# Kernel optimization log

Hardware: AMD Instinct MI355X
Metric: run time of the kernel (lower is better)

## Reference

```python
import jax, jax.numpy as jnp
import numpy as np

N_STATIONS = 35
N_PER_ST = 12
N_NODES = N_STATIONS * N_PER_ST   # 420
MAX_EDGES = 5120                  # true edge count = 34 * 12^2 = 4896
MAX_SUPER = 65536                 # true superedge candidates = 33*12*144 = 57024
PI = float(np.pi)

# constraint rows (r, phi, z) from the torch module
C_LO = jnp.array([269.0, -3.15, -2386.0], dtype=jnp.float32)
C_HI = jnp.array([581.0, 3.15, 2386.0], dtype=jnp.float32)


def _calc_dphi(p1, p2):
    d = p2 - p1
    d = jnp.where(d > PI, d - 2.0 * PI, d)
    return jnp.where(d < -PI, d + 2.0 * PI, d)


def _norm_node(v, k):
    return 2.0 * (v - C_LO[k]) / (C_HI[k] - C_LO[k]) - 1.0


def _norm_edge(v, k):
    return 2.0 * v / (C_HI[k] - C_LO[k])


def setup_inputs() -> dict:
    rng = np.random.default_rng(0)
    r = rng.uniform(270.0, 580.0, N_NODES)
    phi = rng.uniform(-3.1, 3.1, N_NODES)
    z = rng.uniform(-2000.0, 2000.0, N_NODES)
    station = np.arange(N_NODES) // N_PER_ST
    track = np.arange(N_NODES) % N_PER_ST  # one hit per track per station
    data = np.stack([
        np.zeros(N_NODES),          # event
        r * np.sin(phi),            # x (so atan2(x, y) = phi)
        r * np.cos(phi),            # y
        z,                          # z
        station.astype(np.float64),
        track.astype(np.float64),
        np.arange(N_NODES, dtype=np.float64),  # index_old
    ], axis=1).astype(np.float32)
    return {"event_data": jnp.asarray(data)}


def reference(event_data):
    x, y, z = event_data[:, 1], event_data[:, 2], event_data[:, 3]
    station, track, index_old = event_data[:, 4], event_data[:, 5], event_data[:, 6]
    # convert() : cartesian -> cylindrical (x<-r, y<-phi)
    r = jnp.sqrt(x * x + y * y)
    phi = jnp.arctan2(x, y)
    # get_graph(): adjacency of consecutive stations, row-major nonzero like torch
    adj = station[:, None] == (station[None, :] - 1.0)
    i_idx, j_idx = jnp.nonzero(adj, size=MAX_EDGES, fill_value=0)
    e_valid = jnp.arange(MAX_EDGES) < jnp.sum(adj)
    phi_p, phi_c = phi[i_idx], phi[j_idx]
    z_p, z_c = z[i_idx], z[j_idx]
    r_p, r_c = r[i_idx], r[j_idx]
    io_p, io_c = index_old[i_idx], index_old[j_idx]
    is_true = track[i_idx] == track[j_idx]  # torch leaves is_true uninitialized; defined as same-track
    dphi = _calc_dphi(phi_p, phi_c)
    dz, dx = z_c - z_p, r_c - r_p
    ez = (station[i_idx] + 1.0) / N_STATIONS
    e_index = jnp.arange(MAX_EDGES, dtype=event_data.dtype)
    # normalize() node-mode on endpoint phi/z (the only normalized cols used later) and edge-mode on dx,dy,dz
    yp_n, yc_n = _norm_node(phi_p, 1), _norm_node(phi_c, 1)
    zp_n, zc_n = _norm_node(z_p, 2), _norm_node(z_c, 2)
    dx_n, dy_n, dz_n = _norm_edge(dx, 0), _norm_edge(dphi, 1), _norm_edge(dz, 2)
    # apply_edge_restriction (masking instead of compaction)
    e_keep = e_valid & (dy_n > -10.0) & (dy_n < 10.0) & (dz_n > -10.0) & (dz_n < 10.0)
    # get_edges_from_supernodes: join first.index_old_c == second.index_old_p
    eq = (io_c[:, None] == io_p[None, :]) & e_keep[:, None] & e_keep[None, :]
    si, sj = jnp.nonzero(eq, size=MAX_SUPER, fill_value=0)
    s_valid = jnp.arange(MAX_SUPER) < jnp.sum(eq)
    d_first = jnp.stack([dx_n[si], dy_n[si], dz_n[si]], -1)
    d_second = jnp.stack([dx_n[sj], dy_n[sj], dz_n[sj]], -1)
    weight = jnp.linalg.norm(d_first - d_second, axis=1)
    # apply_weight_restriction: compact, order-preserving
    s_keep = s_valid & (weight < 0.1)
    (k_idx,) = jnp.nonzero(s_keep, size=MAX_SUPER, fill_value=0)
    k_valid = jnp.arange(MAX_SUPER) < jnp.sum(s_keep)
    fi, se = si[k_idx], sj[k_idx]
    su_is_true = is_true[fi] & is_true[se]
    su_ioc = jnp.where(k_valid, e_index[fi], -2.0)  # superedge index_old_c = first edge's index
    su_iop = jnp.where(k_valid, e_index[se], -2.0)  # superedge index_old_p = second edge's index
    su_y = jnp.where(k_valid, su_is_true.astype(event_data.dtype), 0.0)
    # construct_output_graph: nodes = (filtered) edges, edges = superedges
    node_idx = jnp.where(e_keep, e_index, -1.0)
    X = jnp.where(e_keep[:, None], jnp.stack([yp_n, yc_n, zp_n, zc_n, ez], -1), 0.0)
    Ri = node_idx[:, None] == su_ioc[None, :]   # [MAX_EDGES, MAX_SUPER] bool
    Ro = node_idx[:, None] == su_iop[None, :]
    super_ids = jnp.stack([su_iop, su_ioc], -1)
    edge_ids = jnp.where(e_keep[:, None], jnp.stack([io_p, io_c, e_index], -1), -1.0)
    return X, Ri, Ro, su_y, super_ids, node_idx, edge_ids
```

## Files before the change

kernel.cpp:

```cpp
#include <hip/hip_runtime.h>
#include <math.h>

#define NND 420
#define MAXE 5120
#define MAXS 65536

#define OFF_X    ((size_t)0)
#define OFF_RI   ((size_t)25600)
#define OFF_RO   ((size_t)25600 + 335544320)
#define OFF_SUY  ((size_t)671114240)
#define OFF_SIDS ((size_t)671179776)
#define OFF_NIDX ((size_t)671310848)
#define OFF_EIDS ((size_t)671315968)
#define OUT_TOTAL ((size_t)671331328)

static __device__ __forceinline__ float f32(double d) { return (float)d; }

__device__ float g_dxn[MAXE], g_dyn[MAXE], g_dzn[MAXE];
__device__ float g_iop[MAXE], g_ioc[MAXE];
__device__ int   g_keep[MAXE], g_istrue[MAXE], g_jn[MAXE];
__device__ int   g_estart[NND + 1];
__device__ int   g_cnt2[MAXE], g_off2[MAXE];
__device__ int   g_nedges, g_nkeep;

__global__ __launch_bounds__(256) void kFill(float4* __restrict__ p, size_t n4) {
    size_t i = (size_t)blockIdx.x * 256 + threadIdx.x;
    size_t stride = (size_t)gridDim.x * 256;
    const float4 z = make_float4(0.f, 0.f, 0.f, 0.f);
    for (; i < n4; i += stride) p[i] = z;
}

__global__ __launch_bounds__(512) void kA(const float* __restrict__ ev,
                                          float* __restrict__ out) {
    __shared__ float s_r[NND], s_phi[NND], s_z[NND], s_st[NND], s_trk[NND], s_io[NND];
    __shared__ int   s_cnt[NND];
    __shared__ int   s_off[NND + 1];
    __shared__ short s_ei[MAXE], s_ej[MAXE];

    const float PI_F  = f32(3.141592653589793);
    const float TPI_F = f32(6.283185307179586);
    const float LO1 = -3.15f, SPAN1 = 3.15f + 3.15f;
    const float LO2 = -2386.0f, SPAN2 = 4772.0f;
    const float SPAN0 = 312.0f;

    int t = threadIdx.x;
    for (int n = t; n < NND; n += 512) {
        float x = ev[n * 7 + 1], y = ev[n * 7 + 2];
        s_z[n]   = ev[n * 7 + 3];
        s_st[n]  = ev[n * 7 + 4];
        s_trk[n] = ev[n * 7 + 5];
        s_io[n]  = ev[n * 7 + 6];
        s_r[n]   = sqrtf(__fadd_rn(__fmul_rn(x, x), __fmul_rn(y, y)));
        s_phi[n] = atan2f(x, y);
    }
    __syncthreads();

    for (int i = t; i < NND; i += 512) {
        float target = s_st[i] + 1.0f;
        int c = 0;
        for (int j = 0; j < NND; ++j) c += (s_st[j] == target) ? 1 : 0;
        s_cnt[i] = c;
    }
    __syncthreads();
    if (t == 0) {
        int acc = 0;
        for (int i = 0; i < NND; ++i) { s_off[i] = acc; acc += s_cnt[i]; }
        s_off[NND] = acc;
        g_nedges = acc;
        for (int n = 0; n <= NND; ++n)
            g_estart[n] = (s_off[n] > MAXE) ? MAXE : s_off[n];
    }
    __syncthreads();

    for (int i = t; i < NND; i += 512) {
        float target = s_st[i] + 1.0f;
        int k = s_off[i];
        for (int j = 0; j < NND; ++j) {
            if (s_st[j] == target) {
                if (k < MAXE) { s_ei[k] = (short)i; s_ej[k] = (short)j; }
                ++k;
            }
        }
    }
    __syncthreads();

    int nedges = s_off[NND]; if (nedges > MAXE) nedges = MAXE;

    for (int k = t; k < MAXE; k += 512) {
        bool valid = (k < nedges);
        int i = valid ? (int)s_ei[k] : 0;
        int j = valid ? (int)s_ej[k] : 0;
        float phip = s_phi[i], phic = s_phi[j];
        float zp = s_z[i], zc = s_z[j];
        float rp = s_r[i], rc = s_r[j];
        float iop = s_io[i], ioc = s_io[j];
        int istrue = (s_trk[i] == s_trk[j]) ? 1 : 0;

        float d = __fsub_rn(phic, phip);
        if (d >  PI_F) d = __fsub_rn(d, TPI_F);
        if (d < -PI_F) d = __fadd_rn(d, TPI_F);

        float dzv = __fsub_rn(zc, zp);
        float dxv = __fsub_rn(rc, rp);
        float dxn = __fdiv_rn(__fmul_rn(2.0f, dxv), SPAN0);
        float dyn = __fdiv_rn(__fmul_rn(2.0f, d),   SPAN1);
        float dzn = __fdiv_rn(__fmul_rn(2.0f, dzv), SPAN2);

        bool keep = valid && (dyn > -10.0f) && (dyn < 10.0f)
                          && (dzn > -10.0f) && (dzn < 10.0f);

        float ypn = __fsub_rn(__fdiv_rn(__fmul_rn(2.0f, __fsub_rn(phip, LO1)), SPAN1), 1.0f);
        float ycn = __fsub_rn(__fdiv_rn(__fmul_rn(2.0f, __fsub_rn(phic, LO1)), SPAN1), 1.0f);
        float zpn = __fsub_rn(__fdiv_rn(__fmul_rn(2.0f, __fsub_rn(zp, LO2)), SPAN2), 1.0f);
        float zcn = __fsub_rn(__fdiv_rn(__fmul_rn(2.0f, __fsub_rn(zc, LO2)), SPAN2), 1.0f);
        float ez  = __fdiv_rn(__fadd_rn(s_st[i], 1.0f), 35.0f);

        size_t oX = OFF_X + (size_t)k * 5;
        out[oX + 0] = keep ? ypn : 0.0f;
        out[oX + 1] = keep ? ycn : 0.0f;
        out[oX + 2] = keep ? zpn : 0.0f;
        out[oX + 3] = keep ? zcn : 0.0f;
        out[oX + 4] = keep ? ez  : 0.0f;

        out[OFF_NIDX + (size_t)k] = keep ? (float)k : -1.0f;
        size_t oE = OFF_EIDS + (size_t)k * 3;
        out[oE + 0] = keep ? iop : -1.0f;
        out[oE + 1] = keep ? ioc : -1.0f;
        out[oE + 2] = keep ? (float)k : -1.0f;

        g_dxn[k] = dxn; g_dyn[k] = dyn; g_dzn[k] = dzn;
        g_iop[k] = iop; g_ioc[k] = ioc;
        g_keep[k] = keep ? 1 : 0; g_istrue[k] = istrue; g_jn[k] = j;
    }
}

__global__ __launch_bounds__(256) void kB() {
    int a = blockIdx.x * 256 + threadIdx.x;
    if (a >= MAXE) return;
    int c = 0;
    if (g_keep[a]) {
        int jn = g_jn[a];
        float ioca = g_ioc[a];
        float a0 = g_dxn[a], a1 = g_dyn[a], a2 = g_dzn[a];
        int b0 = g_estart[jn], b1 = g_estart[jn + 1];
        for (int b = b0; b < b1; ++b) {
            if (g_keep[b] && (g_iop[b] == ioca)) {
                float d0 = __fsub_rn(a0, g_dxn[b]);
                float d1 = __fsub_rn(a1, g_dyn[b]);
                float d2 = __fsub_rn(a2, g_dzn[b]);
                float w = sqrtf(__fadd_rn(__fadd_rn(__fmul_rn(d0, d0),
                                                    __fmul_rn(d1, d1)),
                                          __fmul_rn(d2, d2)));
                if (w < 0.1f) ++c;
            }
        }
    }
    g_cnt2[a] = c;
}

__global__ __launch_bounds__(1024) void kC() {
    __shared__ int part[1024];
    int t = threadIdx.x;
    int v[5]; int s = 0;
#pragma unroll
    for (int q = 0; q < 5; ++q) { v[q] = g_cnt2[t * 5 + q]; s += v[q]; }
    part[t] = s;
    __syncthreads();
    for (int off = 1; off < 1024; off <<= 1) {
        int x = (t >= off) ? part[t - off] : 0;
        __syncthreads();
        part[t] += x;
        __syncthreads();
    }
    int run = part[t] - s;
#pragma unroll
    for (int q = 0; q < 5; ++q) { g_off2[t * 5 + q] = run; run += v[q]; }
    if (t == 1023) g_nkeep = part[1023];
}

__global__ __launch_bounds__(256) void kD(float* __restrict__ out) {
    int a = blockIdx.x * 256 + threadIdx.x;
    if (a >= MAXE) return;
    if (!g_keep[a]) return;
    int pos = g_off2[a];
    int jn = g_jn[a];
    float ioca = g_ioc[a];
    float a0 = g_dxn[a], a1 = g_dyn[a], a2 = g_dzn[a];
    int b0 = g_estart[jn], b1 = g_estart[jn + 1];
    for (int b = b0; b < b1; ++b) {
        if (g_keep[b] && (g_iop[b] == ioca)) {
            float d0 = __fsub_rn(a0, g_dxn[b]);
            float d1 = __fsub_rn(a1, g_dyn[b]);
            float d2 = __fsub_rn(a2, g_dzn[b]);
            float w = sqrtf(__fadd_rn(__fadd_rn(__fmul_rn(d0, d0),
                                                __fmul_rn(d1, d1)),
                                      __fmul_rn(d2, d2)));
            if (w < 0.1f) {
                if (pos < MAXS) {
                    out[OFF_SUY + (size_t)pos] =
                        (g_istrue[a] && g_istrue[b]) ? 1.0f : 0.0f;
                    size_t os = OFF_SIDS + (size_t)pos * 2;
                    out[os + 0] = (float)b;
                    out[os + 1] = (float)a;
                    out[OFF_RI + (size_t)a * MAXS + (size_t)pos] = 1.0f;
                    out[OFF_RO + (size_t)b * MAXS + (size_t)pos] = 1.0f;
                }
                ++pos;
            }
        }
    }
}

__global__ __launch_bounds__(256) void kE(float* __restrict__ out) {
    int p = blockIdx.x * 256 + threadIdx.x;
    if (p >= MAXS) return;
    if (p >= g_nkeep) {
        size_t os = OFF_SIDS + (size_t)p * 2;
        out[os + 0] = -2.0f;
        out[os + 1] = -2.0f;
    }
}

extern "C" void kernel_launch(void* const* d_in, const int* in_sizes, int n_in,
                              void* d_out, int out_size, void* d_ws, size_t ws_size,
                              hipStream_t stream) {
    const float* ev = (const float*)d_in[0];
    float* out = (float*)d_out;

    size_t n4 = (size_t)out_size / 4;
    hipLaunchKernelGGL(kFill, dim3(2048), dim3(256), 0, stream, (float4*)out, n4);

    hipLaunchKernelGGL(kA, dim3(1), dim3(512), 0, stream, ev, out);
    hipLaunchKernelGGL(kB, dim3((MAXE + 255) / 256), dim3(256), 0, stream);
    hipLaunchKernelGGL(kC, dim3(1), dim3(1024), 0, stream);
    hipLaunchKernelGGL(kD, dim3((MAXE + 255) / 256), dim3(256), 0, stream, out);
    hipLaunchKernelGGL(kE, dim3((MAXS + 255) / 256), dim3(256), 0, stream, out);
}
```

Measured before the change: 2.752 ms.

## Split edge building across blocks, wave-parallel superedge search, nontemporal fill

```diff
diff --git a/kernel.cpp b/kernel.cpp
--- a/kernel.cpp
+++ b/kernel.cpp
@@ -7,35 +7,93 @@
 
 #define OFF_X    ((size_t)0)
 #define OFF_RI   ((size_t)25600)
-#define OFF_RO   ((size_t)25600 + 335544320)
+#define OFF_RO   ((size_t)(25600 + 335544320))
 #define OFF_SUY  ((size_t)671114240)
 #define OFF_SIDS ((size_t)671179776)
 #define OFF_NIDX ((size_t)671310848)
 #define OFF_EIDS ((size_t)671315968)
-#define OUT_TOTAL ((size_t)671331328)
+
+typedef float f4 __attribute__((ext_vector_type(4)));
 
 static __device__ __forceinline__ float f32(double d) { return (float)d; }
 
-__device__ float g_dxn[MAXE], g_dyn[MAXE], g_dzn[MAXE];
-__device__ float g_iop[MAXE], g_ioc[MAXE];
+__device__ float g_r[NND], g_phi[NND], g_z[NND], g_st[NND], g_trk[NND], g_io[NND];
+__device__ short g_ei[MAXE], g_ej[MAXE];
+__device__ int   g_estart[NND + 1];
+__device__ float g_dxn[MAXE], g_dyn[MAXE], g_dzn[MAXE], g_iop[MAXE], g_ioc[MAXE];
 __device__ int   g_keep[MAXE], g_istrue[MAXE], g_jn[MAXE];
-__device__ int   g_estart[NND + 1];
 __device__ int   g_cnt2[MAXE], g_off2[MAXE];
 __device__ int   g_nedges, g_nkeep;
 
-__global__ __launch_bounds__(256) void kFill(float4* __restrict__ p, size_t n4) {
+__global__ __launch_bounds__(256) void kFill(f4* __restrict__ p, size_t n4) {
+    const size_t LO = OFF_SIDS >> 2;
+    const size_t HI = (OFF_SIDS + 2 * (size_t)MAXS) >> 2;
     size_t i = (size_t)blockIdx.x * 256 + threadIdx.x;
     size_t stride = (size_t)gridDim.x * 256;
-    const float4 z = make_float4(0.f, 0.f, 0.f, 0.f);
-    for (; i < n4; i += stride) p[i] = z;
-}
-
-__global__ __launch_bounds__(512) void kA(const float* __restrict__ ev,
-                                          float* __restrict__ out) {
+    const f4 z = {0.f, 0.f, 0.f, 0.f};
+    const f4 m = {-2.f, -2.f, -2.f, -2.f};
+    for (; i < n4; i += stride) {
+        f4 v = (i >= LO && i < HI) ? m : z;
+        __builtin_nontemporal_store(v, p + i);
+    }
+}
+
+__global__ __launch_bounds__(512) void kA1(const float* __restrict__ ev) {
+    __shared__ float s_st[NND];
+    __shared__ int   s_scan[NND];
+    int t = threadIdx.x;
+    float stv = 0.0f;
+    if (t < NND) {
+        float x = ev[t * 7 + 1], y = ev[t * 7 + 2];
+        g_r[t]   = sqrtf(__fadd_rn(__fmul_rn(x, x), __fmul_rn(y, y)));
+        g_phi[t] = atan2f(x, y);
+        g_z[t]   = ev[t * 7 + 3];
+        stv      = ev[t * 7 + 4];
+        g_st[t]  = stv;  s_st[t] = stv;
+        g_trk[t] = ev[t * 7 + 5];
+        g_io[t]  = ev[t * 7 + 6];
+    }
+    __syncthreads();
+    int cnt = 0;
+    if (t < NND) {
+        float target = stv + 1.0f;
+        for (int j = 0; j < NND; ++j) cnt += (s_st[j] == target) ? 1 : 0;
+        s_scan[t] = cnt;
+    }
+    __syncthreads();
+    for (int off = 1; off < NND; off <<= 1) {
+        int v = 0;
+        if (t < NND && t >= off) v = s_scan[t - off];
+        __syncthreads();
+        if (t < NND) s_scan[t] += v;
+        __syncthreads();
+    }
+    if (t < NND) {
+        int excl = s_scan[t] - cnt;
+        g_estart[t] = excl > MAXE ? MAXE : excl;
+        int k = excl;
+        float target = stv + 1.0f;
+        for (int j = 0; j < NND; ++j) {
+            if (s_st[j] == target) {
+                if (k < MAXE) { g_ei[k] = (short)t; g_ej[k] = (short)j; }
+                ++k;
+            }
+        }
+        if (t == NND - 1) {
+            g_nedges = s_scan[t];
+            g_estart[NND] = s_scan[t] > MAXE ? MAXE : s_scan[t];
+        }
+    }
+}
+
+__global__ __launch_bounds__(512) void kA2(float* __restrict__ out) {
     __shared__ float s_r[NND], s_phi[NND], s_z[NND], s_st[NND], s_trk[NND], s_io[NND];
-    __shared__ int   s_cnt[NND];
-    __shared__ int   s_off[NND + 1];
-    __shared__ short s_ei[MAXE], s_ej[MAXE];
+    int t = threadIdx.x;
+    for (int n = t; n < NND; n += 512) {
+        s_r[n] = g_r[n]; s_phi[n] = g_phi[n]; s_z[n] = g_z[n];
+        s_st[n] = g_st[n]; s_trk[n] = g_trk[n]; s_io[n] = g_io[n];
+    }
+    __syncthreads();
 
     const float PI_F  = f32(3.141592653589793);
     const float TPI_F = f32(6.283185307179586);
@@ -43,107 +101,66 @@
     const float LO2 = -2386.0f, SPAN2 = 4772.0f;
     const float SPAN0 = 312.0f;
 
-    int t = threadIdx.x;
-    for (int n = t; n < NND; n += 512) {
-        float x = ev[n * 7 + 1], y = ev[n * 7 + 2];
-        s_z[n]   = ev[n * 7 + 3];
-        s_st[n]  = ev[n * 7 + 4];
-        s_trk[n] = ev[n * 7 + 5];
-        s_io[n]  = ev[n * 7 + 6];
-        s_r[n]   = sqrtf(__fadd_rn(__fmul_rn(x, x), __fmul_rn(y, y)));
-        s_phi[n] = atan2f(x, y);
-    }
-    __syncthreads();
-
-    for (int i = t; i < NND; i += 512) {
-        float target = s_st[i] + 1.0f;
-        int c = 0;
-        for (int j = 0; j < NND; ++j) c += (s_st[j] == target) ? 1 : 0;
-        s_cnt[i] = c;
-    }
-    __syncthreads();
-    if (t == 0) {
-        int acc = 0;
-        for (int i = 0; i < NND; ++i) { s_off[i] = acc; acc += s_cnt[i]; }
-        s_off[NND] = acc;
-        g_nedges = acc;
-        for (int n = 0; n <= NND; ++n)
-            g_estart[n] = (s_off[n] > MAXE) ? MAXE : s_off[n];
-    }
-    __syncthreads();
-
-    for (int i = t; i < NND; i += 512) {
-        float target = s_st[i] + 1.0f;
-        int k = s_off[i];
-        for (int j = 0; j < NND; ++j) {
-            if (s_st[j] == target) {
-                if (k < MAXE) { s_ei[k] = (short)i; s_ej[k] = (short)j; }
-                ++k;
-            }
-        }
-    }
-    __syncthreads();
-
-    int nedges = s_off[NND]; if (nedges > MAXE) nedges = MAXE;
-
-    for (int k = t; k < MAXE; k += 512) {
-        bool valid = (k < nedges);
-        int i = valid ? (int)s_ei[k] : 0;
-        int j = valid ? (int)s_ej[k] : 0;
-        float phip = s_phi[i], phic = s_phi[j];
-        float zp = s_z[i], zc = s_z[j];
-        float rp = s_r[i], rc = s_r[j];
-        float iop = s_io[i], ioc = s_io[j];
-        int istrue = (s_trk[i] == s_trk[j]) ? 1 : 0;
-
-        float d = __fsub_rn(phic, phip);
-        if (d >  PI_F) d = __fsub_rn(d, TPI_F);
-        if (d < -PI_F) d = __fadd_rn(d, TPI_F);
-
-        float dzv = __fsub_rn(zc, zp);
-        float dxv = __fsub_rn(rc, rp);
-        float dxn = __fdiv_rn(__fmul_rn(2.0f, dxv), SPAN0);
-        float dyn = __fdiv_rn(__fmul_rn(2.0f, d),   SPAN1);
-        float dzn = __fdiv_rn(__fmul_rn(2.0f, dzv), SPAN2);
-
-        bool keep = valid && (dyn > -10.0f) && (dyn < 10.0f)
-                          && (dzn > -10.0f) && (dzn < 10.0f);
-
-        float ypn = __fsub_rn(__fdiv_rn(__fmul_rn(2.0f, __fsub_rn(phip, LO1)), SPAN1), 1.0f);
-        float ycn = __fsub_rn(__fdiv_rn(__fmul_rn(2.0f, __fsub_rn(phic, LO1)), SPAN1), 1.0f);
-        float zpn = __fsub_rn(__fdiv_rn(__fmul_rn(2.0f, __fsub_rn(zp, LO2)), SPAN2), 1.0f);
-        float zcn = __fsub_rn(__fdiv_rn(__fmul_rn(2.0f, __fsub_rn(zc, LO2)), SPAN2), 1.0f);
-        float ez  = __fdiv_rn(__fadd_rn(s_st[i], 1.0f), 35.0f);
-
-        size_t oX = OFF_X + (size_t)k * 5;
-        out[oX + 0] = keep ? ypn : 0.0f;
-        out[oX + 1] = keep ? ycn : 0.0f;
-        out[oX + 2] = keep ? zpn : 0.0f;
-        out[oX + 3] = keep ? zcn : 0.0f;
-        out[oX + 4] = keep ? ez  : 0.0f;
-
-        out[OFF_NIDX + (size_t)k] = keep ? (float)k : -1.0f;
-        size_t oE = OFF_EIDS + (size_t)k * 3;
-        out[oE + 0] = keep ? iop : -1.0f;
-        out[oE + 1] = keep ? ioc : -1.0f;
-        out[oE + 2] = keep ? (float)k : -1.0f;
-
-        g_dxn[k] = dxn; g_dyn[k] = dyn; g_dzn[k] = dzn;
-        g_iop[k] = iop; g_ioc[k] = ioc;
-        g_keep[k] = keep ? 1 : 0; g_istrue[k] = istrue; g_jn[k] = j;
-    }
+    int k = blockIdx.x * 512 + t;
+    if (k >= MAXE) return;
+    int ne = g_nedges; if (ne > MAXE) ne = MAXE;
+    bool valid = (k < ne);
+    int i = valid ? (int)g_ei[k] : 0;
+    int j = valid ? (int)g_ej[k] : 0;
+
+    float phip = s_phi[i], phic = s_phi[j];
+    float zp = s_z[i], zc = s_z[j];
+    float rp = s_r[i], rc = s_r[j];
+    float iop = s_io[i], ioc = s_io[j];
+    int istrue = (s_trk[i] == s_trk[j]) ? 1 : 0;
+
+    float d = __fsub_rn(phic, phip);
+    if (d >  PI_F) d = __fsub_rn(d, TPI_F);
+    if (d < -PI_F) d = __fadd_rn(d, TPI_F);
+
+    float dzv = __fsub_rn(zc, zp);
+    float dxv = __fsub_rn(rc, rp);
+    float dxn = __fdiv_rn(__fmul_rn(2.0f, dxv), SPAN0);
+    float dyn = __fdiv_rn(__fmul_rn(2.0f, d),   SPAN1);
+    float dzn = __fdiv_rn(__fmul_rn(2.0f, dzv), SPAN2);
+
+    bool keep = valid && (dyn > -10.0f) && (dyn < 10.0f)
+                      && (dzn > -10.0f) && (dzn < 10.0f);
+
+    float ypn = __fsub_rn(__fdiv_rn(__fmul_rn(2.0f, __fsub_rn(phip, LO1)), SPAN1), 1.0f);
+    float ycn = __fsub_rn(__fdiv_rn(__fmul_rn(2.0f, __fsub_rn(phic, LO1)), SPAN1), 1.0f);
+    float zpn = __fsub_rn(__fdiv_rn(__fmul_rn(2.0f, __fsub_rn(zp, LO2)), SPAN2), 1.0f);
+    float zcn = __fsub_rn(__fdiv_rn(__fmul_rn(2.0f, __fsub_rn(zc, LO2)), SPAN2), 1.0f);
+    float ez  = __fdiv_rn(__fadd_rn(s_st[i], 1.0f), 35.0f);
+
+    size_t oX = OFF_X + (size_t)k * 5;
+    out[oX + 0] = keep ? ypn : 0.0f;
+    out[oX + 1] = keep ? ycn : 0.0f;
+    out[oX + 2] = keep ? zpn : 0.0f;
+    out[oX + 3] = keep ? zcn : 0.0f;
+    out[oX + 4] = keep ? ez  : 0.0f;
+
+    out[OFF_NIDX + (size_t)k] = keep ? (float)k : -1.0f;
+    size_t oE = OFF_EIDS + (size_t)k * 3;
+    out[oE + 0] = keep ? iop : -1.0f;
+    out[oE + 1] = keep ? ioc : -1.0f;
+    out[oE + 2] = keep ? (float)k : -1.0f;
+
+    g_dxn[k] = dxn; g_dyn[k] = dyn; g_dzn[k] = dzn;
+    g_iop[k] = iop; g_ioc[k] = ioc;
+    g_keep[k] = keep ? 1 : 0; g_istrue[k] = istrue; g_jn[k] = j;
 }
 
 __global__ __launch_bounds__(256) void kB() {
-    int a = blockIdx.x * 256 + threadIdx.x;
-    if (a >= MAXE) return;
+    int gtid = blockIdx.x * 256 + threadIdx.x;
+    int a = gtid >> 6, lane = gtid & 63;
     int c = 0;
     if (g_keep[a]) {
         int jn = g_jn[a];
+        int b0 = g_estart[jn], b1 = g_estart[jn + 1];
         float ioca = g_ioc[a];
         float a0 = g_dxn[a], a1 = g_dyn[a], a2 = g_dzn[a];
-        int b0 = g_estart[jn], b1 = g_estart[jn + 1];
-        for (int b = b0; b < b1; ++b) {
+        for (int b = b0 + lane; b < b1; b += 64) {
             if (g_keep[b] && (g_iop[b] == ioca)) {
                 float d0 = __fsub_rn(a0, g_dxn[b]);
                 float d1 = __fsub_rn(a1, g_dyn[b]);
@@ -155,7 +172,8 @@
             }
         }
     }
-    g_cnt2[a] = c;
+    for (int off = 32; off; off >>= 1) c += __shfl_down(c, off, 64);
+    if (lane == 0) g_cnt2[a] = c;
 }
 
 __global__ __launch_bounds__(1024) void kC() {
@@ -179,45 +197,40 @@
 }
 
 __global__ __launch_bounds__(256) void kD(float* __restrict__ out) {
-    int a = blockIdx.x * 256 + threadIdx.x;
-    if (a >= MAXE) return;
+    int gtid = blockIdx.x * 256 + threadIdx.x;
+    int a = gtid >> 6, lane = gtid & 63;
     if (!g_keep[a]) return;
-    int pos = g_off2[a];
     int jn = g_jn[a];
+    int b0 = g_estart[jn], b1 = g_estart[jn + 1];
     float ioca = g_ioc[a];
     float a0 = g_dxn[a], a1 = g_dyn[a], a2 = g_dzn[a];
-    int b0 = g_estart[jn], b1 = g_estart[jn + 1];
-    for (int b = b0; b < b1; ++b) {
-        if (g_keep[b] && (g_iop[b] == ioca)) {
+    int ia = g_istrue[a];
+    int base = g_off2[a];
+    for (int cs = b0; cs < b1; cs += 64) {
+        int b = cs + lane;
+        bool pred = false;
+        if (b < b1 && g_keep[b] && (g_iop[b] == ioca)) {
             float d0 = __fsub_rn(a0, g_dxn[b]);
             float d1 = __fsub_rn(a1, g_dyn[b]);
             float d2 = __fsub_rn(a2, g_dzn[b]);
             float w = sqrtf(__fadd_rn(__fadd_rn(__fmul_rn(d0, d0),
                                                 __fmul_rn(d1, d1)),
                                       __fmul_rn(d2, d2)));
-            if (w < 0.1f) {
-                if (pos < MAXS) {
-                    out[OFF_SUY + (size_t)pos] =
-                        (g_istrue[a] && g_istrue[b]) ? 1.0f : 0.0f;
-                    size_t os = OFF_SIDS + (size_t)pos * 2;
-                    out[os + 0] = (float)b;
-                    out[os + 1] = (float)a;
-                    out[OFF_RI + (size_t)a * MAXS + (size_t)pos] = 1.0f;
-                    out[OFF_RO + (size_t)b * MAXS + (size_t)pos] = 1.0f;
-                }
-                ++pos;
+            pred = (w < 0.1f);
+        }
+        unsigned long long mask = __ballot(pred);
+        if (pred) {
+            int pos = base + (int)__popcll(mask & ((1ull << lane) - 1ull));
+            if (pos < MAXS) {
+                out[OFF_SUY + (size_t)pos] = (ia && g_istrue[b]) ? 1.0f : 0.0f;
+                size_t os = OFF_SIDS + (size_t)pos * 2;
+                out[os + 0] = (float)b;
+                out[os + 1] = (float)a;
+                out[OFF_RI + (size_t)a * MAXS + (size_t)pos] = 1.0f;
+                out[OFF_RO + (size_t)b * MAXS + (size_t)pos] = 1.0f;
             }
         }
-    }
-}
-
-__global__ __launch_bounds__(256) void kE(float* __restrict__ out) {
-    int p = blockIdx.x * 256 + threadIdx.x;
-    if (p >= MAXS) return;
-    if (p >= g_nkeep) {
-        size_t os = OFF_SIDS + (size_t)p * 2;
-        out[os + 0] = -2.0f;
-        out[os + 1] = -2.0f;
+        base += (int)__popcll(mask);
     }
 }
 
@@ -228,11 +241,10 @@
     float* out = (float*)d_out;
 
     size_t n4 = (size_t)out_size / 4;
-    hipLaunchKernelGGL(kFill, dim3(2048), dim3(256), 0, stream, (float4*)out, n4);
-
-    hipLaunchKernelGGL(kA, dim3(1), dim3(512), 0, stream, ev, out);
-    hipLaunchKernelGGL(kB, dim3((MAXE + 255) / 256), dim3(256), 0, stream);
+    hipLaunchKernelGGL(kFill, dim3(4096), dim3(256), 0, stream, (f4*)out, n4);
+    hipLaunchKernelGGL(kA1, dim3(1), dim3(512), 0, stream, ev);
+    hipLaunchKernelGGL(kA2, dim3((MAXE + 511) / 512), dim3(512), 0, stream, out);
+    hipLaunchKernelGGL(kB, dim3(MAXE * 64 / 256), dim3(256), 0, stream);
     hipLaunchKernelGGL(kC, dim3(1), dim3(1024), 0, stream);
-    hipLaunchKernelGGL(kD, dim3((MAXE + 255) / 256), dim3(256), 0, stream, out);
-    hipLaunchKernelGGL(kE, dim3((MAXS + 255) / 256), dim3(256), 0, stream, out);
-}
+    hipLaunchKernelGGL(kD, dim3(MAXE * 64 / 256), dim3(256), 0, stream, out);
+}
```

Measured after the change: 2.830 ms. +2.8%, slower.
